# Performance work log

Measured on AMD Instinct MI355X. Metric: run time of the kernel, lower is better.

## Reference

```python
import jax, jax.numpy as jnp
import numpy as np

N_NODE, N_REL, EMB, N_NB, N_TYPES, B = 200000, 16, 128, 16, 4, 4096


def setup_inputs() -> dict:
    key = jax.random.key(0)
    ks = jax.random.split(key, 12)
    s = 1.0 / np.sqrt(EMB)
    return {
        "node": jax.random.randint(ks[0], (B,), 0, N_NODE),
        "relation": jax.random.randint(ks[1], (B,), 0, N_REL),
        "adj_node": jax.random.randint(ks[2], (N_NODE, N_NB), 0, N_NODE),
        "adj_rela": jax.random.randint(ks[3], (N_NODE, N_NB), 0, N_REL),
        "node_type": jax.random.randint(ks[4], (N_NODE,), 0, N_TYPES),
        "node_emb": jax.random.normal(ks[5], (N_NODE, EMB), jnp.float32) * s,
        "rela_emb": jax.random.normal(ks[6], (N_REL, EMB), jnp.float32) * s,
        "type_w": jax.random.uniform(ks[7], (N_TYPES, N_TYPES), jnp.float32),
        "Ws0": jax.random.normal(ks[8], (EMB, EMB), jnp.float32) * s,
        "Wn0": jax.random.normal(ks[9], (EMB, EMB), jnp.float32) * s,
        "Ws1": jax.random.normal(ks[10], (EMB, EMB), jnp.float32) * s,
        "Wn1": jax.random.normal(ks[11], (EMB, EMB), jnp.float32) * s,
    }


def _agg(self_v, nb_v, score, Ws, Wn):
    # self_v: [N,E], nb_v: [N,K,E], score: [N,K] (all neighbors valid -> no mask)
    w = jax.nn.softmax(score, axis=-1)
    agg = jnp.einsum("nk,nke->ne", w, nb_v)
    return self_v @ Ws + agg @ Wn


def reference(node, relation, adj_node, adj_rela, node_type, node_emb, rela_emb,
              type_w, Ws0, Wn0, Ws1, Wn1):
    # --- multi-hop neighbor expansion (get_neighbors) ---
    e1 = adj_node[node]                      # [B,16]
    r1 = adj_rela[node]                      # [B,16]
    e2 = adj_node[e1].reshape(B, -1)         # [B,256]
    r2 = adj_rela[e1].reshape(B, -1)         # [B,256]

    # --- prior embeddings with DistMult-style relation pre-transform ---
    rel_vec = rela_emb[relation]             # [B,E]
    ev0 = node_emb[node] * rel_vec                           # [B,E]
    ev1 = node_emb[e1] * rel_vec[:, None, :]                 # [B,16,E]
    ev2 = node_emb[e2] * rel_vec[:, None, :]                 # [B,256,E]

    # --- relation similarity |cosine| (calc_rsim) ---
    rn = rela_emb / jnp.maximum(jnp.linalg.norm(rela_emb, axis=-1, keepdims=True), 1e-8)
    rsim = jnp.abs(rn @ rn.T)                # [R,R]

    t0 = node_type[node]                     # [B]
    t1 = node_type[e1]                       # [B,16]
    t2 = node_type[e2]                       # [B,256]

    # --- iteration i=0, hop 0 ---
    score00 = rsim[relation[:, None], r1] * type_w[t0[:, None], t1]   # [B,16]
    v0 = jax.nn.relu(_agg(ev0, ev1, score00, Ws0, Wn0))               # [B,E]

    # --- iteration i=0, hop 1 ---
    self1 = ev1.reshape(B * N_NB, EMB)
    nb1 = ev2.reshape(B * N_NB, N_NB, EMB)
    tgt1 = jnp.repeat(relation, N_NB)
    score01 = (rsim[tgt1[:, None], r2.reshape(B * N_NB, N_NB)]
               * type_w[t1.reshape(-1)[:, None], t2.reshape(B * N_NB, N_NB)])
    v1 = jax.nn.relu(_agg(self1, nb1, score01, Ws0, Wn0)).reshape(B, N_NB, EMB)

    # --- iteration i=1, hop 0 (last: no activation) ---
    out = _agg(v0, v1, score00, Ws1, Wn1)    # [B,E]

    # post='none'; norm=1 -> L2 normalize
    out = out / jnp.maximum(jnp.linalg.norm(out, axis=-1, keepdims=True), 1e-12)
    return out
```

## Files before the change

### kernel.cpp

```cpp
#include <hip/hip_runtime.h>
#include <math.h>

#define NB   16
#define EMB  128

typedef __bf16 bf16x8 __attribute__((ext_vector_type(8)));
typedef __bf16 bf16x4 __attribute__((ext_vector_type(4)));
typedef float  f32x4  __attribute__((ext_vector_type(4)));
typedef int    i32x4  __attribute__((ext_vector_type(4)));

__global__ __launch_bounds__(256) void pack_w_kernel(
    const float* __restrict__ Ws0, const float* __restrict__ Wn0,
    __bf16* __restrict__ pack)
{
    int idx = blockIdx.x * 256 + threadIdx.x;
    if (idx >= 4096) return;
    int l  = idx & 63;
    int nt = (idx >> 6) & 7;
    int s  = idx >> 9;
    int col = nt * 16 + (l & 15);
    int k0  = s * 32 + (l >> 4) * 8;
    bf16x8 v;
    #pragma unroll
    for (int j = 0; j < 8; ++j) {
        int k = k0 + j;
        float wv = (k < 128) ? Ws0[k * EMB + col] : Wn0[(k - 128) * EMB + col];
        v[j] = (__bf16)wv;
    }
    *(bf16x8*)(pack + idx * 8) = v;
}

__global__ __launch_bounds__(256) void conv_emb_kernel(
    const float* __restrict__ src, __bf16* __restrict__ dst, int n4)
{
    int i = blockIdx.x * 256 + threadIdx.x;
    if (i >= n4) return;
    f32x4 v = ((const f32x4*)src)[i];
    bf16x4 o;
    o[0] = (__bf16)v[0]; o[1] = (__bf16)v[1];
    o[2] = (__bf16)v[2]; o[3] = (__bf16)v[3];
    ((bf16x4*)dst)[i] = o;
}

template<bool BT>
__device__ __forceinline__ f32x4 load_rq(const void* tab, int idx, int q) {
    if constexpr (BT) {
        bf16x4 v = *((const bf16x4*)tab + idx * 32 + q);
        f32x4 r;
        r[0] = (float)v[0]; r[1] = (float)v[1];
        r[2] = (float)v[2]; r[3] = (float)v[3];
        return r;
    } else {
        return *((const f32x4*)tab + idx * 32 + q);
    }
}

template<bool BT>
__global__ __launch_bounds__(256, 4) void gnn_kernel(
    const int* __restrict__ node, const int* __restrict__ relation,
    const int* __restrict__ adj_node, const int* __restrict__ adj_rela,
    const int* __restrict__ node_type, const void* __restrict__ tab,
    const float* __restrict__ rela_emb, const float* __restrict__ type_w,
    const float* __restrict__ Ws1, const float* __restrict__ Wn1,
    const __bf16* __restrict__ packW0,
    float* __restrict__ out)
{
    __shared__ __align__(16) unsigned char Xb[17 * 512];
    __shared__ __align__(16) float sw01[16][16];
    __shared__ __align__(16) int   se2[16][16];
    __shared__ __align__(16) float relv[EMB];
    __shared__ __align__(16) f32x4 red4[8][32];
    __shared__ __align__(16) float y0[EMB];
    __shared__ __align__(16) float y1[EMB];
    __shared__ float sw00[16];
    __shared__ float srsim[16];
    __shared__ float sdij[16], sdrr[16];
    __shared__ int   se1[16], sr1[16], st1[16];

    const int t   = threadIdx.x;
    const int b   = blockIdx.x;
    const int nb0 = node[b];
    const int rel = relation[b];

    if (t < 16) {
        int e1 = adj_node[nb0 * NB + t];
        se1[t] = e1;
        sr1[t] = adj_rela[nb0 * NB + t];
        st1[t] = node_type[e1];
    }
    if (t < EMB) relv[t] = rela_emb[rel * EMB + t];
    {
        int r = t >> 4, c = t & 15;
        float dij = 0.f, drr = 0.f;
        #pragma unroll
        for (int dd = 0; dd < 8; ++dd) {
            int d = dd * 16 + c;
            float a  = rela_emb[rel * EMB + d];
            float bb = rela_emb[r * EMB + d];
            dij = fmaf(a, bb, dij);
            drr = fmaf(bb, bb, drr);
        }
        #pragma unroll
        for (int off = 8; off >= 1; off >>= 1) {
            dij += __shfl_xor(dij, off);
            drr += __shfl_xor(drr, off);
        }
        if (c == 0) { sdij[r] = dij; sdrr[r] = drr; }
    }
    __syncthreads();

    if (t < 16) {
        float nrel = fmaxf(sqrtf(sdrr[rel]), 1e-8f);
        float nr   = fmaxf(sqrtf(sdrr[t]),   1e-8f);
        srsim[t] = fabsf(sdij[t]) / (nr * nrel);
    }
    __syncthreads();

    {
        int k = t >> 4, j = t & 15;
        int e1k = se1[k];
        int e2  = adj_node[e1k * NB + j];
        int r2  = adj_rela[e1k * NB + j];
        int t2  = node_type[e2];
        se2[k][j] = e2;
        float s = srsim[r2] * type_w[st1[k] * 4 + t2];
        float m = s;
        #pragma unroll
        for (int off = 8; off >= 1; off >>= 1) m = fmaxf(m, __shfl_xor(m, off));
        float ex = __expf(s - m);
        float sum = ex;
        #pragma unroll
        for (int off = 8; off >= 1; off >>= 1) sum += __shfl_xor(sum, off);
        sw01[k][j] = ex / sum;
    }
    {
        int t0type = node_type[nb0];
        if (t < 16) {
            float s = srsim[sr1[t]] * type_w[t0type * 4 + st1[t]];
            float m = s;
            #pragma unroll
            for (int off = 8; off >= 1; off >>= 1) m = fmaxf(m, __shfl_xor(m, off));
            float ex = __expf(s - m);
            float sum = ex;
            #pragma unroll
            for (int off = 8; off >= 1; off >>= 1) sum += __shfl_xor(sum, off);
            sw00[t] = ex / sum;
        }
    }
    __syncthreads();

    {
        const int q = t & 31;
        const int g = t >> 5;
        const f32x4 rv4 = *(const f32x4*)&relv[q * 4];
        f32x4 pagg = {0.f, 0.f, 0.f, 0.f};

        for (int kx = 0; kx < 2; ++kx) {
            const int k = g + kx * 8;
            const int swz = (k & 7) << 4;

            const f32x4 sv = load_rq<BT>(tab, se1[k], q);
            const float wk0 = sw00[k];
            pagg += wk0 * sv;
            bf16x4 xs;
            xs[0] = (__bf16)(sv[0] * rv4[0]);
            xs[1] = (__bf16)(sv[1] * rv4[1]);
            xs[2] = (__bf16)(sv[2] * rv4[2]);
            xs[3] = (__bf16)(sv[3] * rv4[3]);
            *(bf16x4*)(Xb + ((k * 512 + q * 8) ^ swz)) = xs;

            i32x4 i0 = *(const i32x4*)&se2[k][0];
            i32x4 i1 = *(const i32x4*)&se2[k][4];
            i32x4 i2 = *(const i32x4*)&se2[k][8];
            i32x4 i3 = *(const i32x4*)&se2[k][12];
            f32x4 w0 = *(const f32x4*)&sw01[k][0];
            f32x4 w1 = *(const f32x4*)&sw01[k][4];
            f32x4 w2 = *(const f32x4*)&sw01[k][8];
            f32x4 w3 = *(const f32x4*)&sw01[k][12];

            f32x4 v0  = load_rq<BT>(tab, i0[0], q);
            f32x4 v1  = load_rq<BT>(tab, i0[1], q);
            f32x4 v2  = load_rq<BT>(tab, i0[2], q);
            f32x4 v3  = load_rq<BT>(tab, i0[3], q);
            f32x4 v4  = load_rq<BT>(tab, i1[0], q);
            f32x4 v5  = load_rq<BT>(tab, i1[1], q);
            f32x4 v6  = load_rq<BT>(tab, i1[2], q);
            f32x4 v7  = load_rq<BT>(tab, i1[3], q);
            f32x4 v8  = load_rq<BT>(tab, i2[0], q);
            f32x4 v9  = load_rq<BT>(tab, i2[1], q);
            f32x4 v10 = load_rq<BT>(tab, i2[2], q);
            f32x4 v11 = load_rq<BT>(tab, i2[3], q);
            f32x4 v12 = load_rq<BT>(tab, i3[0], q);
            f32x4 v13 = load_rq<BT>(tab, i3[1], q);
            f32x4 v14 = load_rq<BT>(tab, i3[2], q);
            f32x4 v15 = load_rq<BT>(tab, i3[3], q);

            f32x4 s01 = w0[0] * v0;  s01 += w0[1] * v1;
            f32x4 s23 = w0[2] * v2;  s23 += w0[3] * v3;
            f32x4 s45 = w1[0] * v4;  s45 += w1[1] * v5;
            f32x4 s67 = w1[2] * v6;  s67 += w1[3] * v7;
            f32x4 s89 = w2[0] * v8;  s89 += w2[1] * v9;
            f32x4 sab = w2[2] * v10; sab += w2[3] * v11;
            f32x4 scd = w3[0] * v12; scd += w3[1] * v13;
            f32x4 sef = w3[2] * v14; sef += w3[3] * v15;
            s01 += s23; s45 += s67; s89 += sab; scd += sef;
            s01 += s45; s89 += scd;
            f32x4 acc = s01 + s89;

            bf16x4 xa;
            xa[0] = (__bf16)(acc[0] * rv4[0]);
            xa[1] = (__bf16)(acc[1] * rv4[1]);
            xa[2] = (__bf16)(acc[2] * rv4[2]);
            xa[3] = (__bf16)(acc[3] * rv4[3]);
            *(bf16x4*)(Xb + ((k * 512 + 256 + q * 8) ^ swz)) = xa;
        }
        red4[g][q] = pagg;
    }
    __syncthreads();
    if (t < 32) {
        f32x4 s = red4[0][t];
        #pragma unroll
        for (int g = 1; g < 8; ++g) s += red4[g][t];
        const f32x4 rv4 = *(const f32x4*)&relv[t * 4];
        const f32x4 ev0 = load_rq<BT>(tab, nb0, t);
        bf16x4 h0s, h0a;
        #pragma unroll
        for (int c = 0; c < 4; ++c) {
            h0s[c] = (__bf16)(ev0[c] * rv4[c]);
            h0a[c] = (__bf16)(s[c]   * rv4[c]);
        }
        *(bf16x4*)(Xb + 16 * 512 + t * 8)       = h0s;
        *(bf16x4*)(Xb + 16 * 512 + 256 + t * 8) = h0a;
    }
    __syncthreads();

    const int w = t >> 6, l = t & 63;
    f32x4 acc00 = {0.f, 0.f, 0.f, 0.f};
    f32x4 acc01 = {0.f, 0.f, 0.f, 0.f};
    f32x4 acc10 = {0.f, 0.f, 0.f, 0.f};
    f32x4 acc11 = {0.f, 0.f, 0.f, 0.f};
    {
        const int row0 = l & 15;
        const int kb   = (l >> 4) * 16;
        const int sw0  = (row0 & 7) << 4;
        #pragma unroll
        for (int s = 0; s < 8; ++s) {
            bf16x8 a0 = *(const bf16x8*)(Xb + ((row0 * 512 + s * 64 + kb) ^ sw0));
            bf16x8 a1 = *(const bf16x8*)(Xb + (16 * 512 + s * 64 + kb));
            bf16x8 b0 = *(const bf16x8*)(packW0 + (((s * 8 + 2 * w) * 64 + l) * 8));
            bf16x8 b1 = *(const bf16x8*)(packW0 + (((s * 8 + 2 * w + 1) * 64 + l) * 8));
            acc00 = __builtin_amdgcn_mfma_f32_16x16x32_bf16(a0, b0, acc00, 0, 0, 0);
            acc01 = __builtin_amdgcn_mfma_f32_16x16x32_bf16(a0, b1, acc01, 0, 0, 0);
            acc10 = __builtin_amdgcn_mfma_f32_16x16x32_bf16(a1, b0, acc10, 0, 0, 0);
            acc11 = __builtin_amdgcn_mfma_f32_16x16x32_bf16(a1, b1, acc11, 0, 0, 0);
        }
    }

    {
        const int rbase = (l >> 4) * 4;
        float s0 = 0.f, s1 = 0.f;
        #pragma unroll
        for (int r = 0; r < 4; ++r) {
            float wk = sw00[rbase + r];
            s0 = fmaf(wk, fmaxf(acc00[r], 0.f), s0);
            s1 = fmaf(wk, fmaxf(acc01[r], 0.f), s1);
        }
        s0 += __shfl_xor(s0, 16); s0 += __shfl_xor(s0, 32);
        s1 += __shfl_xor(s1, 16); s1 += __shfl_xor(s1, 32);
        if (l < 16) {
            int c0 = (2 * w) * 16 + l, c1 = (2 * w + 1) * 16 + l;
            y1[c0] = s0;
            y1[c1] = s1;
            y0[c0] = fmaxf(acc10[0], 0.f);
            y0[c1] = fmaxf(acc11[0], 0.f);
        }
    }
    __syncthreads();

    {
        const int q = t & 31;
        const int g = t >> 5;
        const int d0 = g * 16;
        f32x4 a = {0.f, 0.f, 0.f, 0.f};
        #pragma unroll
        for (int dq = 0; dq < 4; ++dq) {
            f32x4 ys = *(const f32x4*)&y0[d0 + dq * 4];
            f32x4 ya = *(const f32x4*)&y1[d0 + dq * 4];
            #pragma unroll
            for (int jj = 0; jj < 4; ++jj) {
                const int d = d0 + dq * 4 + jj;
                f32x4 ws = *(const f32x4*)(Ws1 + d * EMB + q * 4);
                f32x4 wn = *(const f32x4*)(Wn1 + d * EMB + q * 4);
                a += ys[jj] * ws;
                a += ya[jj] * wn;
            }
        }
        red4[g][q] = a;
    }
    __syncthreads();

    if (t < 32) {
        f32x4 o = red4[0][t];
        #pragma unroll
        for (int g = 1; g < 8; ++g) o += red4[g][t];
        float sq = o[0] * o[0] + o[1] * o[1] + o[2] * o[2] + o[3] * o[3];
        #pragma unroll
        for (int off = 1; off < 32; off <<= 1) sq += __shfl_xor(sq, off);
        float inv = 1.f / fmaxf(sqrtf(sq), 1e-12f);
        o *= inv;
        *(f32x4*)(out + b * EMB + t * 4) = o;
    }
}

extern "C" void kernel_launch(void* const* d_in, const int* in_sizes, int n_in,
                              void* d_out, int out_size, void* d_ws, size_t ws_size,
                              hipStream_t stream) {
    (void)n_in; (void)out_size;
    const int*   node      = (const int*)d_in[0];
    const int*   relation  = (const int*)d_in[1];
    const int*   adj_node  = (const int*)d_in[2];
    const int*   adj_rela  = (const int*)d_in[3];
    const int*   node_type = (const int*)d_in[4];
    const float* node_emb  = (const float*)d_in[5];
    const float* rela_emb  = (const float*)d_in[6];
    const float* type_w    = (const float*)d_in[7];
    const float* Ws0       = (const float*)d_in[8];
    const float* Wn0       = (const float*)d_in[9];
    const float* Ws1       = (const float*)d_in[10];
    const float* Wn1       = (const float*)d_in[11];
    float* out = (float*)d_out;
    const int B     = in_sizes[0];
    const int nnode = in_sizes[5] / EMB;

    __bf16* packW0 = (__bf16*)d_ws;
    __bf16* tabbf  = (__bf16*)((char*)d_ws + 65536);
    const size_t need = 65536 + (size_t)nnode * EMB * 2;

    pack_w_kernel<<<16, 256, 0, stream>>>(Ws0, Wn0, packW0);

    if (ws_size >= need) {
        const int n4 = nnode * EMB / 4;
        conv_emb_kernel<<<(n4 + 255) / 256, 256, 0, stream>>>(node_emb, tabbf, n4);
        gnn_kernel<true><<<B, 256, 0, stream>>>(node, relation, adj_node, adj_rela,
                                                node_type, (const void*)tabbf, rela_emb,
                                                type_w, Ws1, Wn1, packW0, out);
    } else {
        gnn_kernel<false><<<B, 256, 0, stream>>>(node, relation, adj_node, adj_rela,
                                                 node_type, (const void*)node_emb, rela_emb,
                                                 type_w, Ws1, Wn1, packW0, out);
    }
}
```

Baseline: 99.72 us.

## Batch two queries per block and run final layer on MFMA

```diff
diff --git a/kernel.cpp b/kernel.cpp
--- a/kernel.cpp
+++ b/kernel.cpp
@@ -3,6 +3,8 @@
 
 #define NB   16
 #define EMB  128
+#define G    2
+#define XSTRIDE 8704
 
 typedef __bf16 bf16x8 __attribute__((ext_vector_type(8)));
 typedef __bf16 bf16x4 __attribute__((ext_vector_type(4)));
@@ -11,23 +13,46 @@
 
 __global__ __launch_bounds__(256) void pack_w_kernel(
     const float* __restrict__ Ws0, const float* __restrict__ Wn0,
+    const float* __restrict__ Ws1, const float* __restrict__ Wn1,
     __bf16* __restrict__ pack)
 {
     int idx = blockIdx.x * 256 + threadIdx.x;
-    if (idx >= 4096) return;
+    if (idx >= 8192) return;
     int l  = idx & 63;
     int nt = (idx >> 6) & 7;
-    int s  = idx >> 9;
+    int s  = (idx >> 9) & 7;
+    int m  = idx >> 12;
     int col = nt * 16 + (l & 15);
     int k0  = s * 32 + (l >> 4) * 8;
+    const float* Wa = m ? Ws1 : Ws0;
+    const float* Wb = m ? Wn1 : Wn0;
     bf16x8 v;
     #pragma unroll
     for (int j = 0; j < 8; ++j) {
         int k = k0 + j;
-        float wv = (k < 128) ? Ws0[k * EMB + col] : Wn0[(k - 128) * EMB + col];
+        float wv = (k < 128) ? Wa[k * EMB + col] : Wb[(k - 128) * EMB + col];
         v[j] = (__bf16)wv;
     }
-    *(bf16x8*)(pack + idx * 8) = v;
+    *(bf16x8*)(pack + (size_t)idx * 8) = v;
+}
+
+__global__ __launch_bounds__(256) void rsim_kernel(
+    const float* __restrict__ rela_emb, float* __restrict__ rsim)
+{
+    __shared__ float dd[16][16];
+    int t = threadIdx.x, r = t >> 4, c = t & 15;
+    float d = 0.f;
+    #pragma unroll
+    for (int k4 = 0; k4 < 32; ++k4) {
+        f32x4 a = *(const f32x4*)(rela_emb + r * EMB + k4 * 4);
+        f32x4 b = *(const f32x4*)(rela_emb + c * EMB + k4 * 4);
+        d += a[0]*b[0] + a[1]*b[1] + a[2]*b[2] + a[3]*b[3];
+    }
+    dd[r][c] = d;
+    __syncthreads();
+    float nr = fmaxf(sqrtf(dd[r][r]), 1e-8f);
+    float nc = fmaxf(sqrtf(dd[c][c]), 1e-8f);
+    rsim[t] = fabsf(d) / (nr * nc);
 }
 
 __global__ __launch_bounds__(256) void conv_emb_kernel(
@@ -61,82 +86,50 @@
     const int* __restrict__ adj_node, const int* __restrict__ adj_rela,
     const int* __restrict__ node_type, const void* __restrict__ tab,
     const float* __restrict__ rela_emb, const float* __restrict__ type_w,
-    const float* __restrict__ Ws1, const float* __restrict__ Wn1,
-    const __bf16* __restrict__ packW0,
+    const __bf16* __restrict__ packW, const float* __restrict__ rsimg,
     float* __restrict__ out)
 {
-    __shared__ __align__(16) unsigned char Xb[17 * 512];
+    __shared__ __align__(16) unsigned char Xb[G * XSTRIDE];
+    __shared__ __align__(16) unsigned char Yb[16 * 512];
+    __shared__ __align__(16) float scratch[1024];
     __shared__ __align__(16) float sw01[16][16];
     __shared__ __align__(16) int   se2[16][16];
     __shared__ __align__(16) float relv[EMB];
-    __shared__ __align__(16) f32x4 red4[8][32];
-    __shared__ __align__(16) float y0[EMB];
-    __shared__ __align__(16) float y1[EMB];
-    __shared__ float sw00[16];
+    __shared__ float sw00[G][16];
     __shared__ float srsim[16];
-    __shared__ float sdij[16], sdrr[16];
     __shared__ int   se1[16], sr1[16], st1[16];
 
-    const int t   = threadIdx.x;
-    const int b   = blockIdx.x;
-    const int nb0 = node[b];
-    const int rel = relation[b];
-
-    if (t < 16) {
-        int e1 = adj_node[nb0 * NB + t];
-        se1[t] = e1;
-        sr1[t] = adj_rela[nb0 * NB + t];
-        st1[t] = node_type[e1];
-    }
-    if (t < EMB) relv[t] = rela_emb[rel * EMB + t];
+    const int t  = threadIdx.x;
+    const int b0 = blockIdx.x * G;
+
     {
-        int r = t >> 4, c = t & 15;
-        float dij = 0.f, drr = 0.f;
-        #pragma unroll
-        for (int dd = 0; dd < 8; ++dd) {
-            int d = dd * 16 + c;
-            float a  = rela_emb[rel * EMB + d];
-            float bb = rela_emb[r * EMB + d];
-            dij = fmaf(a, bb, dij);
-            drr = fmaf(bb, bb, drr);
-        }
-        #pragma unroll
-        for (int off = 8; off >= 1; off >>= 1) {
-            dij += __shfl_xor(dij, off);
-            drr += __shfl_xor(drr, off);
-        }
-        if (c == 0) { sdij[r] = dij; sdrr[r] = drr; }
-    }
-    __syncthreads();
-
-    if (t < 16) {
-        float nrel = fmaxf(sqrtf(sdrr[rel]), 1e-8f);
-        float nr   = fmaxf(sqrtf(sdrr[t]),   1e-8f);
-        srsim[t] = fabsf(sdij[t]) / (nr * nrel);
-    }
-    __syncthreads();
-
-    {
-        int k = t >> 4, j = t & 15;
-        int e1k = se1[k];
-        int e2  = adj_node[e1k * NB + j];
-        int r2  = adj_rela[e1k * NB + j];
-        int t2  = node_type[e2];
-        se2[k][j] = e2;
-        float s = srsim[r2] * type_w[st1[k] * 4 + t2];
-        float m = s;
-        #pragma unroll
-        for (int off = 8; off >= 1; off >>= 1) m = fmaxf(m, __shfl_xor(m, off));
-        float ex = __expf(s - m);
-        float sum = ex;
-        #pragma unroll
-        for (int off = 8; off >= 1; off >>= 1) sum += __shfl_xor(sum, off);
-        sw01[k][j] = ex / sum;
-    }
-    {
-        int t0type = node_type[nb0];
+        f32x4 z = {0.f, 0.f, 0.f, 0.f};
+        *(f32x4*)(Yb + t * 16)        = z;
+        *(f32x4*)(Yb + 4096 + t * 16) = z;
+    }
+
+    for (int e = 0; e < G; ++e) {
+        const int nb0 = node[b0 + e];
+        const int rel = relation[b0 + e];
+
         if (t < 16) {
-            float s = srsim[sr1[t]] * type_w[t0type * 4 + st1[t]];
+            int e1 = adj_node[nb0 * NB + t];
+            se1[t] = e1;
+            sr1[t] = adj_rela[nb0 * NB + t];
+            st1[t] = node_type[e1];
+            srsim[t] = rsimg[rel * 16 + t];
+        }
+        if (t < EMB) relv[t] = rela_emb[rel * EMB + t];
+        __syncthreads();
+
+        {
+            int k = t >> 4, j = t & 15;
+            int e1k = se1[k];
+            int e2  = adj_node[e1k * NB + j];
+            int r2  = adj_rela[e1k * NB + j];
+            int t2  = node_type[e2];
+            se2[k][j] = e2;
+            float s = srsim[r2] * type_w[st1[k] * 4 + t2];
             float m = s;
             #pragma unroll
             for (int off = 8; off >= 1; off >>= 1) m = fmaxf(m, __shfl_xor(m, off));
@@ -144,171 +137,200 @@
             float sum = ex;
             #pragma unroll
             for (int off = 8; off >= 1; off >>= 1) sum += __shfl_xor(sum, off);
-            sw00[t] = ex / sum;
-        }
-    }
-    __syncthreads();
-
-    {
-        const int q = t & 31;
-        const int g = t >> 5;
-        const f32x4 rv4 = *(const f32x4*)&relv[q * 4];
-        f32x4 pagg = {0.f, 0.f, 0.f, 0.f};
-
-        for (int kx = 0; kx < 2; ++kx) {
-            const int k = g + kx * 8;
-            const int swz = (k & 7) << 4;
-
-            const f32x4 sv = load_rq<BT>(tab, se1[k], q);
-            const float wk0 = sw00[k];
-            pagg += wk0 * sv;
-            bf16x4 xs;
-            xs[0] = (__bf16)(sv[0] * rv4[0]);
-            xs[1] = (__bf16)(sv[1] * rv4[1]);
-            xs[2] = (__bf16)(sv[2] * rv4[2]);
-            xs[3] = (__bf16)(sv[3] * rv4[3]);
-            *(bf16x4*)(Xb + ((k * 512 + q * 8) ^ swz)) = xs;
-
-            i32x4 i0 = *(const i32x4*)&se2[k][0];
-            i32x4 i1 = *(const i32x4*)&se2[k][4];
-            i32x4 i2 = *(const i32x4*)&se2[k][8];
-            i32x4 i3 = *(const i32x4*)&se2[k][12];
-            f32x4 w0 = *(const f32x4*)&sw01[k][0];
-            f32x4 w1 = *(const f32x4*)&sw01[k][4];
-            f32x4 w2 = *(const f32x4*)&sw01[k][8];
-            f32x4 w3 = *(const f32x4*)&sw01[k][12];
-
-            f32x4 v0  = load_rq<BT>(tab, i0[0], q);
-            f32x4 v1  = load_rq<BT>(tab, i0[1], q);
-            f32x4 v2  = load_rq<BT>(tab, i0[2], q);
-            f32x4 v3  = load_rq<BT>(tab, i0[3], q);
-            f32x4 v4  = load_rq<BT>(tab, i1[0], q);
-            f32x4 v5  = load_rq<BT>(tab, i1[1], q);
-            f32x4 v6  = load_rq<BT>(tab, i1[2], q);
-            f32x4 v7  = load_rq<BT>(tab, i1[3], q);
-            f32x4 v8  = load_rq<BT>(tab, i2[0], q);
-            f32x4 v9  = load_rq<BT>(tab, i2[1], q);
-            f32x4 v10 = load_rq<BT>(tab, i2[2], q);
-            f32x4 v11 = load_rq<BT>(tab, i2[3], q);
-            f32x4 v12 = load_rq<BT>(tab, i3[0], q);
-            f32x4 v13 = load_rq<BT>(tab, i3[1], q);
-            f32x4 v14 = load_rq<BT>(tab, i3[2], q);
-            f32x4 v15 = load_rq<BT>(tab, i3[3], q);
-
-            f32x4 s01 = w0[0] * v0;  s01 += w0[1] * v1;
-            f32x4 s23 = w0[2] * v2;  s23 += w0[3] * v3;
-            f32x4 s45 = w1[0] * v4;  s45 += w1[1] * v5;
-            f32x4 s67 = w1[2] * v6;  s67 += w1[3] * v7;
-            f32x4 s89 = w2[0] * v8;  s89 += w2[1] * v9;
-            f32x4 sab = w2[2] * v10; sab += w2[3] * v11;
-            f32x4 scd = w3[0] * v12; scd += w3[1] * v13;
-            f32x4 sef = w3[2] * v14; sef += w3[3] * v15;
-            s01 += s23; s45 += s67; s89 += sab; scd += sef;
-            s01 += s45; s89 += scd;
-            f32x4 acc = s01 + s89;
-
-            bf16x4 xa;
-            xa[0] = (__bf16)(acc[0] * rv4[0]);
-            xa[1] = (__bf16)(acc[1] * rv4[1]);
-            xa[2] = (__bf16)(acc[2] * rv4[2]);
-            xa[3] = (__bf16)(acc[3] * rv4[3]);
-            *(bf16x4*)(Xb + ((k * 512 + 256 + q * 8) ^ swz)) = xa;
-        }
-        red4[g][q] = pagg;
-    }
-    __syncthreads();
-    if (t < 32) {
-        f32x4 s = red4[0][t];
-        #pragma unroll
-        for (int g = 1; g < 8; ++g) s += red4[g][t];
-        const f32x4 rv4 = *(const f32x4*)&relv[t * 4];
-        const f32x4 ev0 = load_rq<BT>(tab, nb0, t);
-        bf16x4 h0s, h0a;
-        #pragma unroll
-        for (int c = 0; c < 4; ++c) {
-            h0s[c] = (__bf16)(ev0[c] * rv4[c]);
-            h0a[c] = (__bf16)(s[c]   * rv4[c]);
-        }
-        *(bf16x4*)(Xb + 16 * 512 + t * 8)       = h0s;
-        *(bf16x4*)(Xb + 16 * 512 + 256 + t * 8) = h0a;
-    }
-    __syncthreads();
+            sw01[k][j] = ex / sum;
+        }
+        {
+            int t0type = node_type[nb0];
+            if (t < 16) {
+                float s = srsim[sr1[t]] * type_w[t0type * 4 + st1[t]];
+                float m = s;
+                #pragma unroll
+                for (int off = 8; off >= 1; off >>= 1) m = fmaxf(m, __shfl_xor(m, off));
+                float ex = __expf(s - m);
+                float sum = ex;
+                #pragma unroll
+                for (int off = 8; off >= 1; off >>= 1) sum += __shfl_xor(sum, off);
+                sw00[e][t] = ex / sum;
+            }
+        }
+        __syncthreads();
+
+        unsigned char* Xe = Xb + e * XSTRIDE;
+        {
+            const int q = t & 31;
+            const int g = t >> 5;
+            const f32x4 rv4 = *(const f32x4*)&relv[q * 4];
+            f32x4 pagg = {0.f, 0.f, 0.f, 0.f};
+
+            for (int kx = 0; kx < 2; ++kx) {
+                const int k = g + kx * 8;
+                const int swz = (k & 7) << 4;
+
+                const f32x4 sv = load_rq<BT>(tab, se1[k], q);
+                pagg += sw00[e][k] * sv;
+                bf16x4 xs;
+                xs[0] = (__bf16)(sv[0] * rv4[0]);
+                xs[1] = (__bf16)(sv[1] * rv4[1]);
+                xs[2] = (__bf16)(sv[2] * rv4[2]);
+                xs[3] = (__bf16)(sv[3] * rv4[3]);
+                *(bf16x4*)(Xe + ((k * 512 + q * 8) ^ swz)) = xs;
+
+                i32x4 i0 = *(const i32x4*)&se2[k][0];
+                i32x4 i1 = *(const i32x4*)&se2[k][4];
+                i32x4 i2 = *(const i32x4*)&se2[k][8];
+                i32x4 i3 = *(const i32x4*)&se2[k][12];
+                f32x4 w0 = *(const f32x4*)&sw01[k][0];
+                f32x4 w1 = *(const f32x4*)&sw01[k][4];
+                f32x4 w2 = *(const f32x4*)&sw01[k][8];
+                f32x4 w3 = *(const f32x4*)&sw01[k][12];
+
+                f32x4 v0  = load_rq<BT>(tab, i0[0], q);
+                f32x4 v1  = load_rq<BT>(tab, i0[1], q);
+                f32x4 v2  = load_rq<BT>(tab, i0[2], q);
+                f32x4 v3  = load_rq<BT>(tab, i0[3], q);
+                f32x4 v4  = load_rq<BT>(tab, i1[0], q);
+                f32x4 v5  = load_rq<BT>(tab, i1[1], q);
+                f32x4 v6  = load_rq<BT>(tab, i1[2], q);
+                f32x4 v7  = load_rq<BT>(tab, i1[3], q);
+                f32x4 v8  = load_rq<BT>(tab, i2[0], q);
+                f32x4 v9  = load_rq<BT>(tab, i2[1], q);
+                f32x4 v10 = load_rq<BT>(tab, i2[2], q);
+                f32x4 v11 = load_rq<BT>(tab, i2[3], q);
+                f32x4 v12 = load_rq<BT>(tab, i3[0], q);
+                f32x4 v13 = load_rq<BT>(tab, i3[1], q);
+                f32x4 v14 = load_rq<BT>(tab, i3[2], q);
+                f32x4 v15 = load_rq<BT>(tab, i3[3], q);
+
+                f32x4 s01 = w0[0] * v0;  s01 += w0[1] * v1;
+                f32x4 s23 = w0[2] * v2;  s23 += w0[3] * v3;
+                f32x4 s45 = w1[0] * v4;  s45 += w1[1] * v5;
+                f32x4 s67 = w1[2] * v6;  s67 += w1[3] * v7;
+                f32x4 s89 = w2[0] * v8;  s89 += w2[1] * v9;
+                f32x4 sab = w2[2] * v10; sab += w2[3] * v11;
+                f32x4 scd = w3[0] * v12; scd += w3[1] * v13;
+                f32x4 sef = w3[2] * v14; sef += w3[3] * v15;
+                s01 += s23; s45 += s67; s89 += sab; scd += sef;
+                s01 += s45; s89 += scd;
+                f32x4 acc = s01 + s89;
+
+                bf16x4 xa;
+                xa[0] = (__bf16)(acc[0] * rv4[0]);
+                xa[1] = (__bf16)(acc[1] * rv4[1]);
+                xa[2] = (__bf16)(acc[2] * rv4[2]);
+                xa[3] = (__bf16)(acc[3] * rv4[3]);
+                *(bf16x4*)(Xe + ((k * 512 + 256 + q * 8) ^ swz)) = xa;
+            }
+            ((f32x4*)scratch)[g * 32 + q] = pagg;
+        }
+        __syncthreads();
+        if (t < 32) {
+            f32x4 s = ((f32x4*)scratch)[t];
+            #pragma unroll
+            for (int g = 1; g < 8; ++g) s += ((f32x4*)scratch)[g * 32 + t];
+            const f32x4 rv4 = *(const f32x4*)&relv[t * 4];
+            const f32x4 ev0 = load_rq<BT>(tab, nb0, t);
+            bf16x4 h0s, h0a;
+            #pragma unroll
+            for (int c = 0; c < 4; ++c) {
+                h0s[c] = (__bf16)(ev0[c] * rv4[c]);
+                h0a[c] = (__bf16)(s[c]   * rv4[c]);
+            }
+            *(bf16x4*)(Xe + 16 * 512 + t * 8)       = h0s;
+            *(bf16x4*)(Xe + 16 * 512 + 256 + t * 8) = h0a;
+        }
+        __syncthreads();
+    }
 
     const int w = t >> 6, l = t & 63;
-    f32x4 acc00 = {0.f, 0.f, 0.f, 0.f};
-    f32x4 acc01 = {0.f, 0.f, 0.f, 0.f};
-    f32x4 acc10 = {0.f, 0.f, 0.f, 0.f};
-    f32x4 acc11 = {0.f, 0.f, 0.f, 0.f};
+    f32x4 acc[G][2][2];
+    #pragma unroll
+    for (int e = 0; e < G; ++e)
+        #pragma unroll
+        for (int m = 0; m < 2; ++m)
+            #pragma unroll
+            for (int n = 0; n < 2; ++n)
+                acc[e][m][n] = (f32x4){0.f, 0.f, 0.f, 0.f};
     {
         const int row0 = l & 15;
         const int kb   = (l >> 4) * 16;
         const int sw0  = (row0 & 7) << 4;
         #pragma unroll
         for (int s = 0; s < 8; ++s) {
-            bf16x8 a0 = *(const bf16x8*)(Xb + ((row0 * 512 + s * 64 + kb) ^ sw0));
-            bf16x8 a1 = *(const bf16x8*)(Xb + (16 * 512 + s * 64 + kb));
-            bf16x8 b0 = *(const bf16x8*)(packW0 + (((s * 8 + 2 * w) * 64 + l) * 8));
-            bf16x8 b1 = *(const bf16x8*)(packW0 + (((s * 8 + 2 * w + 1) * 64 + l) * 8));
-            acc00 = __builtin_amdgcn_mfma_f32_16x16x32_bf16(a0, b0, acc00, 0, 0, 0);
-            acc01 = __builtin_amdgcn_mfma_f32_16x16x32_bf16(a0, b1, acc01, 0, 0, 0);
-            acc10 = __builtin_amdgcn_mfma_f32_16x16x32_bf16(a1, b0, acc10, 0, 0, 0);
-            acc11 = __builtin_amdgcn_mfma_f32_16x16x32_bf16(a1, b1, acc11, 0, 0, 0);
-        }
-    }
-
-    {
+            bf16x8 bf0 = *(const bf16x8*)(packW + ((s * 8 + 2 * w) * 64 + l) * 8);
+            bf16x8 bf1 = *(const bf16x8*)(packW + ((s * 8 + 2 * w + 1) * 64 + l) * 8);
+            #pragma unroll
+            for (int e = 0; e < G; ++e) {
+                const unsigned char* Xe = Xb + e * XSTRIDE;
+                bf16x8 a0 = *(const bf16x8*)(Xe + ((row0 * 512 + s * 64 + kb) ^ sw0));
+                bf16x8 a1 = *(const bf16x8*)(Xe + (16 * 512 + s * 64 + kb));
+                acc[e][0][0] = __builtin_amdgcn_mfma_f32_16x16x32_bf16(a0, bf0, acc[e][0][0], 0, 0, 0);
+                acc[e][0][1] = __builtin_amdgcn_mfma_f32_16x16x32_bf16(a0, bf1, acc[e][0][1], 0, 0, 0);
+                acc[e][1][0] = __builtin_amdgcn_mfma_f32_16x16x32_bf16(a1, bf0, acc[e][1][0], 0, 0, 0);
+                acc[e][1][1] = __builtin_amdgcn_mfma_f32_16x16x32_bf16(a1, bf1, acc[e][1][1], 0, 0, 0);
+            }
+        }
+    }
+
+    #pragma unroll
+    for (int e = 0; e < G; ++e) {
         const int rbase = (l >> 4) * 4;
         float s0 = 0.f, s1 = 0.f;
         #pragma unroll
         for (int r = 0; r < 4; ++r) {
-            float wk = sw00[rbase + r];
-            s0 = fmaf(wk, fmaxf(acc00[r], 0.f), s0);
-            s1 = fmaf(wk, fmaxf(acc01[r], 0.f), s1);
+            float wk = sw00[e][rbase + r];
+            s0 = fmaf(wk, fmaxf(acc[e][0][0][r], 0.f), s0);
+            s1 = fmaf(wk, fmaxf(acc[e][0][1][r], 0.f), s1);
         }
         s0 += __shfl_xor(s0, 16); s0 += __shfl_xor(s0, 32);
         s1 += __shfl_xor(s1, 16); s1 += __shfl_xor(s1, 32);
         if (l < 16) {
-            int c0 = (2 * w) * 16 + l, c1 = (2 * w + 1) * 16 + l;
-            y1[c0] = s0;
-            y1[c1] = s1;
-            y0[c0] = fmaxf(acc10[0], 0.f);
-            y0[c1] = fmaxf(acc11[0], 0.f);
+            int c0 = 2 * w * 16 + l, c1 = c0 + 16;
+            const int swz = (e & 7) << 4;
+            *(__bf16*)(Yb + ((e * 512 + c0 * 2) ^ swz))         = (__bf16)fmaxf(acc[e][1][0][0], 0.f);
+            *(__bf16*)(Yb + ((e * 512 + c1 * 2) ^ swz))         = (__bf16)fmaxf(acc[e][1][1][0], 0.f);
+            *(__bf16*)(Yb + ((e * 512 + (128 + c0) * 2) ^ swz)) = (__bf16)s0;
+            *(__bf16*)(Yb + ((e * 512 + (128 + c1) * 2) ^ swz)) = (__bf16)s1;
         }
     }
     __syncthreads();
 
     {
-        const int q = t & 31;
-        const int g = t >> 5;
-        const int d0 = g * 16;
-        f32x4 a = {0.f, 0.f, 0.f, 0.f};
-        #pragma unroll
-        for (int dq = 0; dq < 4; ++dq) {
-            f32x4 ys = *(const f32x4*)&y0[d0 + dq * 4];
-            f32x4 ya = *(const f32x4*)&y1[d0 + dq * 4];
-            #pragma unroll
-            for (int jj = 0; jj < 4; ++jj) {
-                const int d = d0 + dq * 4 + jj;
-                f32x4 ws = *(const f32x4*)(Ws1 + d * EMB + q * 4);
-                f32x4 wn = *(const f32x4*)(Wn1 + d * EMB + q * 4);
-                a += ys[jj] * ws;
-                a += ya[jj] * wn;
-            }
-        }
-        red4[g][q] = a;
+        f32x4 h0 = {0.f, 0.f, 0.f, 0.f};
+        f32x4 h1 = {0.f, 0.f, 0.f, 0.f};
+        const int row0 = l & 15;
+        const int kb   = (l >> 4) * 16;
+        const int sw0  = (row0 & 7) << 4;
+        const __bf16* packW1 = packW + 32768;
+        #pragma unroll
+        for (int s = 0; s < 8; ++s) {
+            bf16x8 a   = *(const bf16x8*)(Yb + ((row0 * 512 + s * 64 + kb) ^ sw0));
+            bf16x8 bf0 = *(const bf16x8*)(packW1 + ((s * 8 + 2 * w) * 64 + l) * 8);
+            bf16x8 bf1 = *(const bf16x8*)(packW1 + ((s * 8 + 2 * w + 1) * 64 + l) * 8);
+            h0 = __builtin_amdgcn_mfma_f32_16x16x32_bf16(a, bf0, h0, 0, 0, 0);
+            h1 = __builtin_amdgcn_mfma_f32_16x16x32_bf16(a, bf1, h1, 0, 0, 0);
+        }
+        if (l < 16) {
+            int c0 = 2 * w * 16 + l, c1 = c0 + 16;
+            #pragma unroll
+            for (int e = 0; e < G; ++e) {
+                scratch[e * EMB + c0] = h0[e];
+                scratch[e * EMB + c1] = h1[e];
+            }
+        }
     }
     __syncthreads();
 
-    if (t < 32) {
-        f32x4 o = red4[0][t];
-        #pragma unroll
-        for (int g = 1; g < 8; ++g) o += red4[g][t];
-        float sq = o[0] * o[0] + o[1] * o[1] + o[2] * o[2] + o[3] * o[3];
-        #pragma unroll
-        for (int off = 1; off < 32; off <<= 1) sq += __shfl_xor(sq, off);
+    if (t < 64 * G) {
+        int e  = t >> 6;
+        int c2 = (t & 63) * 2;
+        float a  = scratch[e * EMB + c2];
+        float bb = scratch[e * EMB + c2 + 1];
+        float sq = a * a + bb * bb;
+        #pragma unroll
+        for (int off = 1; off < 64; off <<= 1) sq += __shfl_xor(sq, off);
         float inv = 1.f / fmaxf(sqrtf(sq), 1e-12f);
-        o *= inv;
-        *(f32x4*)(out + b * EMB + t * 4) = o;
+        out[(b0 + e) * EMB + c2]     = a * inv;
+        out[(b0 + e) * EMB + c2 + 1] = bb * inv;
     }
 }
 
@@ -332,21 +354,24 @@
     const int B     = in_sizes[0];
     const int nnode = in_sizes[5] / EMB;
 
-    __bf16* packW0 = (__bf16*)d_ws;
-    __bf16* tabbf  = (__bf16*)((char*)d_ws + 65536);
-    const size_t need = 65536 + (size_t)nnode * EMB * 2;
-
-    pack_w_kernel<<<16, 256, 0, stream>>>(Ws0, Wn0, packW0);
-
+    __bf16* packW = (__bf16*)d_ws;
+    float*  rsimg = (float*)((char*)d_ws + 131072);
+    __bf16* tabbf = (__bf16*)((char*)d_ws + 132096);
+    const size_t need = 132096 + (size_t)nnode * EMB * 2;
+
+    pack_w_kernel<<<32, 256, 0, stream>>>(Ws0, Wn0, Ws1, Wn1, packW);
+    rsim_kernel<<<1, 256, 0, stream>>>(rela_emb, rsimg);
+
+    const int grid = B / G;
     if (ws_size >= need) {
         const int n4 = nnode * EMB / 4;
         conv_emb_kernel<<<(n4 + 255) / 256, 256, 0, stream>>>(node_emb, tabbf, n4);
-        gnn_kernel<true><<<B, 256, 0, stream>>>(node, relation, adj_node, adj_rela,
-                                                node_type, (const void*)tabbf, rela_emb,
-                                                type_w, Ws1, Wn1, packW0, out);
+        gnn_kernel<true><<<grid, 256, 0, stream>>>(node, relation, adj_node, adj_rela,
+                                                   node_type, (const void*)tabbf, rela_emb,
+                                                   type_w, packW, rsimg, out);
     } else {
-        gnn_kernel<false><<<B, 256, 0, stream>>>(node, relation, adj_node, adj_rela,
-                                                 node_type, (const void*)node_emb, rela_emb,
-                                                 type_w, Ws1, Wn1, packW0, out);
-    }
-}
+        gnn_kernel<false><<<grid, 256, 0, stream>>>(node, relation, adj_node, adj_rela,
+                                                    node_type, (const void*)node_emb, rela_emb,
+                                                    type_w, packW, rsimg, out);
+    }
+}
```

Measured after the change: 99.11 us. No clear change (-0.6%).
